# Kernel optimization log

Measured on AMD Instinct MI355X. Metric: run time of the kernel, lower is better.

## Reference

```python
import jax, jax.numpy as jnp
import numpy as np

TOP_K = 2  # routing_method: renormalize top-2 (topk then softmax over selected logits)


def setup_inputs() -> dict:
    key = jax.random.key(0)
    ks = jax.random.split(key, 5)
    T, H, I, E = 4096, 1024, 4096, 8
    return {
        "hidden_states": jax.random.normal(ks[0], (T, H), jnp.float32),
        "router_logits": jax.random.normal(ks[1], (T, E), jnp.float32),
        "W_gate": jax.random.normal(ks[2], (E, H, I), jnp.float32) * 0.02,  # w1
        "W_up": jax.random.normal(ks[3], (E, H, I), jnp.float32) * 0.02,   # w3
        "W_down": jax.random.normal(ks[4], (E, I, H), jnp.float32) * 0.02, # w2
    }


def reference(hidden_states, router_logits, W_gate, W_up, W_down):
    # Routing: top-k logits, renormalize with softmax over selected logits.
    top_vals, top_idx = jax.lax.top_k(router_logits, TOP_K)        # [T, K]
    routing_weights = jax.nn.softmax(top_vals, axis=-1)            # [T, K]

    E = W_gate.shape[0]
    out = jnp.zeros_like(hidden_states)                            # [T, H]
    for e in range(E):  # fixed small expert loop (structurally distinct weights)
        # combine weight for expert e per token (0 if not routed here)
        w_e = jnp.sum(jnp.where(top_idx == e, routing_weights, 0.0), axis=-1)  # [T]
        gate = hidden_states @ W_gate[e]                           # [T, I]
        up = hidden_states @ W_up[e]                               # [T, I]
        y = (jax.nn.silu(gate) * up) @ W_down[e]                   # [T, H]
        out = out + w_e[:, None] * y
    return out
```

## Files before the change

kernel.cpp:

```cpp
#include <hip/hip_runtime.h>

typedef float    f32x4 __attribute__((ext_vector_type(4)));
typedef _Float16 f16x8 __attribute__((ext_vector_type(8)));
typedef _Float16 f16x4 __attribute__((ext_vector_type(4)));

#define T_TOK 4096
#define HD    1024
#define ID    4096
#define NE    8
#define TOTP  (2*T_TOK)
#define MAXT1 72
#define MAXT2 40

#define WS_CNT   0
#define WS_FILL  64
#define WS_OFF   128
#define WS_TOT   192
#define WS_TOT2  196
#define WS_TEXP  256
#define WS_TM0   (256 + 4*MAXT1)
#define WS_TEXP2 (256 + 8*MAXT1)
#define WS_TM02  (256 + 8*MAXT1 + 4*MAXT2)
#define WS_TOPE  2048
#define WS_TOPW  (WS_TOPE + 4*TOTP)
#define WS_PAIR  (WS_TOPW + 4*TOTP)
#define WS_ACT   ((size_t)1 << 20)
constexpr size_t WS_YBUF = WS_ACT  + 2ull*TOTP*ID;
constexpr size_t WS_HS16 = WS_YBUF + 2ull*TOTP*HD;
constexpr size_t WS_WG16 = WS_HS16 + 2ull*T_TOK*HD;
constexpr size_t WS_WU16 = WS_WG16 + 2ull*NE*HD*ID;
constexpr size_t WS_WD16 = WS_WU16 + 2ull*NE*HD*ID;
constexpr size_t WS_YB   = WS_WG16;

__device__ __forceinline__ void gll16(const void* g, void* l) {
  __builtin_amdgcn_global_load_lds(
      (const __attribute__((address_space(1))) unsigned int*)g,
      (__attribute__((address_space(3))) unsigned int*)l, 16, 0, 0);
}

#define WAITV(N) do { \
    asm volatile("s_waitcnt vmcnt(" #N ")" ::: "memory"); \
    __builtin_amdgcn_sched_barrier(0); \
  } while (0)

__device__ __forceinline__ int lofs64(int row, int g8) {
  return row * 64 + ((g8 ^ (row & 7)) << 3);
}

__global__ void k_router(const float* __restrict__ logits, char* __restrict__ ws) {
  int t = blockIdx.x * blockDim.x + threadIdx.x;
  if (t >= T_TOK) return;
  float v0 = -1e30f, v1 = -1e30f; int i0 = 0, i1 = 0;
  #pragma unroll
  for (int e = 0; e < NE; ++e) {
    float v = logits[t * NE + e];
    if (v > v0)      { v1 = v0; i1 = i0; v0 = v; i0 = e; }
    else if (v > v1) { v1 = v;  i1 = e; }
  }
  float w0 = 1.f / (1.f + __expf(v1 - v0));
  ((int*)(ws + WS_TOPE))[2*t]   = i0;
  ((int*)(ws + WS_TOPE))[2*t+1] = i1;
  ((float*)(ws + WS_TOPW))[2*t]   = w0;
  ((float*)(ws + WS_TOPW))[2*t+1] = 1.f - w0;
  atomicAdd(&((int*)(ws + WS_CNT))[i0], 1);
  atomicAdd(&((int*)(ws + WS_CNT))[i1], 1);
}

__global__ void k_prefix(char* __restrict__ ws) {
  if (threadIdx.x != 0 || blockIdx.x != 0) return;
  const int* cnt = (const int*)(ws + WS_CNT);
  int* off   = (int*)(ws + WS_OFF);
  int* texp  = (int*)(ws + WS_TEXP);
  int* tm0   = (int*)(ws + WS_TM0);
  int* texp2 = (int*)(ws + WS_TEXP2);
  int* tm02  = (int*)(ws + WS_TM02);
  int run = 0, t1 = 0, t2 = 0;
  for (int e = 0; e < NE; ++e) {
    off[e] = run;
    int ne = cnt[e];
    for (int i = 0; i < ne; i += 128) { texp[t1] = e; tm0[t1] = i; ++t1; }
    for (int i = 0; i < ne; i += 256) { texp2[t2] = e; tm02[t2] = i; ++t2; }
    run += ne;
  }
  off[NE] = run;
  *(int*)(ws + WS_TOT)  = t1;
  *(int*)(ws + WS_TOT2) = t2;
}

__global__ void k_scatter(char* __restrict__ ws) {
  int t = blockIdx.x * blockDim.x + threadIdx.x;
  if (t >= T_TOK) return;
  const int* tope = (const int*)(ws + WS_TOPE);
  const int* off  = (const int*)(ws + WS_OFF);
  int* fill = (int*)(ws + WS_FILL);
  int* pair = (int*)(ws + WS_PAIR);
  #pragma unroll
  for (int s = 0; s < 2; ++s) {
    int id = 2*t + s;
    int e = tope[id];
    int pos = off[e] + atomicAdd(&fill[e], 1);
    pair[pos] = id;
  }
}

__global__ void k_hscvt(const float* __restrict__ src, _Float16* __restrict__ dst) {
  int i = blockIdx.x * blockDim.x + threadIdx.x;
  f32x4 v = ((const f32x4*)src)[i];
  f16x4 o;
  #pragma unroll
  for (int j = 0; j < 4; ++j) o[j] = (_Float16)v[j];
  ((f16x4*)dst)[i] = o;
}

__global__ __launch_bounds__(256) void k_wtrans(const float* __restrict__ src,
                                                _Float16* __restrict__ dst,
                                                int K, int N) {
  const int e = blockIdx.z;
  const int n0 = blockIdx.x * 64, k0 = blockIdx.y * 64;
  const float* s = src + (size_t)e * K * N;
  _Float16* d = dst + (size_t)e * (size_t)K * N;
  __shared__ _Float16 t[64][68];
  const int tx = threadIdx.x & 15, ty = threadIdx.x >> 4;
  #pragma unroll
  for (int it = 0; it < 4; ++it) {
    int k = k0 + it*16 + ty;
    f32x4 v = *(const f32x4*)&s[(size_t)k * N + n0 + tx*4];
    #pragma unroll
    for (int j = 0; j < 4; ++j) t[tx*4 + j][it*16 + ty] = (_Float16)v[j];
  }
  __syncthreads();
  #pragma unroll
  for (int it = 0; it < 4; ++it) {
    int n = it*16 + ty;
    *(f16x4*)&d[(size_t)(n0 + n) * K + k0 + tx*4] = *(const f16x4*)&t[n][tx*4];
  }
}

__global__ __launch_bounds__(512, 2) void k_gemm1(
    const _Float16* __restrict__ hs16, const _Float16* __restrict__ WgT,
    const _Float16* __restrict__ WuT, char* __restrict__ ws) {
  const int s = blockIdx.y;
  if (s >= *(const int*)(ws + WS_TOT2)) return;
  const int e    = ((const int*)(ws + WS_TEXP2))[s];
  const int m0   = ((const int*)(ws + WS_TM02))[s];
  const int offE = ((const int*)(ws + WS_OFF))[e];
  const int nE   = ((const int*)(ws + WS_CNT))[e];
  _Float16* __restrict__ act = (_Float16*)(ws + WS_ACT);
  const int n0 = blockIdx.x * 128;
  const int tid = threadIdx.x, lane = tid & 63, wid = tid >> 6;

  __shared__ __align__(16) _Float16 sm[2 * 32768];

  const int r8 = lane >> 3;
  const int q64 = (((lane & 7) ^ r8) << 3);
  const int* __restrict__ pairp = (const int*)(ws + WS_PAIR);
  const _Float16 *aP[4], *gP[2], *uP[2];
  #pragma unroll
  for (int c = 0; c < 4; ++c) {
    int mm = m0 + 32*wid + 8*c + r8;
    int tok = (mm < nE) ? (pairp[offE + mm] >> 1) : 0;
    aP[c] = hs16 + (size_t)tok * HD + q64;
  }
  #pragma unroll
  for (int c = 0; c < 2; ++c) {
    size_t col = (size_t)e * ID + (n0 + 16*wid + 8*c + r8);
    gP[c] = WgT + col * HD + q64;
    uP[c] = WuT + col * HD + q64;
  }

  auto stage8 = [&](int buf, int kt) {
    _Float16* base = sm + buf * 32768;
    const int ko = kt * 64;
    #pragma unroll
    for (int c = 0; c < 4; ++c)
      gll16(aP[c] + ko, base + (32*wid + 8*c) * 64);
    #pragma unroll
    for (int c = 0; c < 2; ++c) {
      gll16(gP[c] + ko, base + 16384 + (16*wid + 8*c) * 64);
      gll16(uP[c] + ko, base + 24576 + (16*wid + 8*c) * 64);
    }
  };

  const int wr = wid >> 2, wc = wid & 3;
  const int l15 = lane & 15, l4 = lane >> 4;
  f32x4 accg[8][2] = {}, accu[8][2] = {};

  auto computeKK = [&](int buf, int kk) {
    const _Float16* b0 = sm + buf * 32768;
    f16x8 afr[8], bg[2], bu[2];
    #pragma unroll
    for (int i = 0; i < 8; ++i) {
      const int row = 128*wr + 16*i + l15;
      afr[i] = *(const f16x8*)&b0[lofs64(row, kk*4 + l4)];
    }
    #pragma unroll
    for (int j = 0; j < 2; ++j) {
      const int row = 32*wc + 16*j + l15;
      bg[j] = *(const f16x8*)&b0[16384 + lofs64(row, kk*4 + l4)];
      bu[j] = *(const f16x8*)&b0[24576 + lofs64(row, kk*4 + l4)];
    }
    __builtin_amdgcn_s_setprio(1);
    #pragma unroll
    for (int i = 0; i < 8; ++i)
      #pragma unroll
      for (int j = 0; j < 2; ++j) {
        accg[i][j] = __builtin_amdgcn_mfma_f32_16x16x32_f16(afr[i], bg[j], accg[i][j], 0, 0, 0);
        accu[i][j] = __builtin_amdgcn_mfma_f32_16x16x32_f16(afr[i], bu[j], accu[i][j], 0, 0, 0);
      }
    __builtin_amdgcn_s_setprio(0);
  };

  const int KT = HD / 64;
  stage8(0, 0);
  WAITV(0);
  __builtin_amdgcn_s_barrier();
  for (int t = 0; t < KT; ++t) {
    const int cur = t & 1;
    if (t + 1 < KT) stage8(cur ^ 1, t + 1);
    computeKK(cur, 0);
    computeKK(cur, 1);
    WAITV(0);
    __builtin_amdgcn_s_barrier();
  }

  #pragma unroll
  for (int i = 0; i < 8; ++i)
    #pragma unroll
    for (int r = 0; r < 4; ++r) {
      const int mm = m0 + 128*wr + 16*i + 4*l4 + r;
      if (mm < nE) {
        const size_t prow = (size_t)(offE + mm) * ID;
        #pragma unroll
        for (int j = 0; j < 2; ++j) {
          float g = accg[i][j][r], u = accu[i][j][r];
          float sv = g / (1.f + __expf(-g)) * u;
          act[prow + n0 + 32*wc + 16*j + l15] = (_Float16)sv;
        }
      }
    }
}

__global__ __launch_bounds__(512, 2) void k_gemm2(const _Float16* __restrict__ WdT,
                                                  char* __restrict__ ws) {
  const int s = blockIdx.y;
  if (s >= *(const int*)(ws + WS_TOT2)) return;
  const int e    = ((const int*)(ws + WS_TEXP2))[s];
  const int m0   = ((const int*)(ws + WS_TM02))[s];
  const int offE = ((const int*)(ws + WS_OFF))[e];
  const int nE   = ((const int*)(ws + WS_CNT))[e];
  const int h    = blockIdx.z;
  const int kbase = h * (ID / 4);
  const int* __restrict__ pair = (const int*)(ws + WS_PAIR);
  const _Float16* __restrict__ act = (const _Float16*)(ws + WS_ACT);
  _Float16* __restrict__ yb = (_Float16*)(ws + WS_YB) + (size_t)h * TOTP * HD;
  const int n0 = blockIdx.x * 256;
  const int tid = threadIdx.x, lane = tid & 63, wid = tid >> 6;

  __shared__ __align__(16) _Float16 sm[2 * 32768];

  const int r8 = lane >> 3;
  const int q64 = (((lane & 7) ^ r8) << 3);
  const _Float16 *aP[4], *bP[4];
  #pragma unroll
  for (int c = 0; c < 4; ++c) {
    int mm = m0 + 32*wid + 8*c + r8;
    int p = (mm < nE) ? (offE + mm) : offE;
    aP[c] = act + (size_t)p * ID + kbase + q64;
  }
  #pragma unroll
  for (int c = 0; c < 4; ++c)
    bP[c] = WdT + ((size_t)e * HD + (n0 + 32*wid + 8*c + r8)) * ID + kbase + q64;

  auto stage8 = [&](int buf, int kt) {
    _Float16* base = sm + buf * 32768;
    const int ko = kt * 64;
    #pragma unroll
    for (int c = 0; c < 4; ++c)
      gll16(aP[c] + ko, base + (32*wid + 8*c) * 64);
    #pragma unroll
    for (int c = 0; c < 4; ++c)
      gll16(bP[c] + ko, base + 16384 + (32*wid + 8*c) * 64);
  };

  const int wr = wid >> 2, wc = wid & 3;
  const int l15 = lane & 15, l4 = lane >> 4;
  f32x4 acc[8][4] = {};

  auto computeKK = [&](int buf, int kk) {
    const _Float16* b0 = sm + buf * 32768;
    f16x8 afr[8], bfr[4];
    #pragma unroll
    for (int i = 0; i < 8; ++i)
      afr[i] = *(const f16x8*)&b0[lofs64(128*wr + 16*i + l15, kk*4 + l4)];
    #pragma unroll
    for (int j = 0; j < 4; ++j)
      bfr[j] = *(const f16x8*)&b0[16384 + lofs64(64*wc + 16*j + l15, kk*4 + l4)];
    __builtin_amdgcn_s_setprio(1);
    #pragma unroll
    for (int i = 0; i < 8; ++i)
      #pragma unroll
      for (int j = 0; j < 4; ++j)
        acc[i][j] = __builtin_amdgcn_mfma_f32_16x16x32_f16(afr[i], bfr[j], acc[i][j], 0, 0, 0);
    __builtin_amdgcn_s_setprio(0);
  };

  const int KT = (ID / 4) / 64;
  stage8(0, 0);
  WAITV(0);
  __builtin_amdgcn_s_barrier();
  for (int t = 0; t < KT; ++t) {
    const int cur = t & 1;
    if (t + 1 < KT) stage8(cur ^ 1, t + 1);
    computeKK(cur, 0);
    computeKK(cur, 1);
    WAITV(0);
    __builtin_amdgcn_s_barrier();
  }

  #pragma unroll
  for (int i = 0; i < 8; ++i)
    #pragma unroll
    for (int r = 0; r < 4; ++r) {
      const int mm = m0 + 128*wr + 16*i + 4*l4 + r;
      if (mm < nE) {
        const int id = pair[offE + mm];
        #pragma unroll
        for (int j = 0; j < 4; ++j)
          yb[(size_t)id * HD + n0 + 64*wc + 16*j + l15] = (_Float16)acc[i][j][r];
      }
    }
}

__global__ void k_combine(const char* __restrict__ ws, float* __restrict__ out) {
  const int idx = blockIdx.x * blockDim.x + threadIdx.x;
  const int t = idx >> 7, c = idx & 127;
  const float* topw = (const float*)(ws + WS_TOPW);
  const _Float16* yb = (const _Float16*)(ws + WS_YB);
  float s0[8] = {}, s1[8] = {};
  #pragma unroll
  for (int h = 0; h < 4; ++h) {
    const _Float16* p = yb + (size_t)h * TOTP * HD;
    f16x8 y0 = ((const f16x8*)(p + (size_t)(2*t)     * HD))[c];
    f16x8 y1 = ((const f16x8*)(p + (size_t)(2*t + 1) * HD))[c];
    #pragma unroll
    for (int j = 0; j < 8; ++j) { s0[j] += (float)y0[j]; s1[j] += (float)y1[j]; }
  }
  const float w0 = topw[2*t], w1 = topw[2*t+1];
  f32x4 o0, o1;
  #pragma unroll
  for (int j = 0; j < 4; ++j) {
    o0[j] = w0 * s0[j]     + w1 * s1[j];
    o1[j] = w0 * s0[4 + j] + w1 * s1[4 + j];
  }
  ((f32x4*)out)[2*idx]     = o0;
  ((f32x4*)out)[2*idx + 1] = o1;
}

extern "C" void kernel_launch(void* const* d_in, const int* in_sizes, int n_in,
                              void* d_out, int out_size, void* d_ws, size_t ws_size,
                              hipStream_t stream) {
  const float* hs     = (const float*)d_in[0];
  const float* logits = (const float*)d_in[1];
  const float* Wg     = (const float*)d_in[2];
  const float* Wu     = (const float*)d_in[3];
  const float* Wd     = (const float*)d_in[4];
  char* ws = (char*)d_ws;

  _Float16* hs16 = (_Float16*)(ws + WS_HS16);
  _Float16* wg16 = (_Float16*)(ws + WS_WG16);
  _Float16* wu16 = (_Float16*)(ws + WS_WU16);
  _Float16* wd16 = (_Float16*)(ws + WS_WD16);

  hipMemsetAsync(ws, 0, 256, stream);
  k_router <<<dim3(T_TOK/256), dim3(256), 0, stream>>>(logits, ws);
  k_prefix <<<dim3(1),         dim3(64),  0, stream>>>(ws);
  k_scatter<<<dim3(T_TOK/256), dim3(256), 0, stream>>>(ws);
  k_hscvt  <<<dim3(T_TOK*HD/4/256), dim3(256), 0, stream>>>(hs, hs16);
  k_wtrans <<<dim3(ID/64, HD/64, NE), dim3(256), 0, stream>>>(Wg, wg16, HD, ID);
  k_wtrans <<<dim3(ID/64, HD/64, NE), dim3(256), 0, stream>>>(Wu, wu16, HD, ID);
  k_wtrans <<<dim3(HD/64, ID/64, NE), dim3(256), 0, stream>>>(Wd, wd16, ID, HD);
  k_gemm1  <<<dim3(ID/128, MAXT2),    dim3(512), 0, stream>>>(hs16, wg16, wu16, ws);
  k_gemm2  <<<dim3(HD/256, MAXT2, 4), dim3(512), 0, stream>>>(wd16, ws);
  k_combine<<<dim3(T_TOK*HD/8/256), dim3(256), 0, stream>>>(ws, (float*)d_out);
}
```

Baseline: 479.9 us.

## Use 32x32x16 MFMA in both expert GEMMs and halve gemm2 split-K

Both grouped GEMMs switch from 16x16x32 to 32x32x16 f16 MFMA tiles, with new fragment loads and epilogue index mapping for the 32x32 accumulator layout. Each block keeps the same output tile but issues fewer, larger MFMAs and fewer LDS fragment reads. Separately, the down-projection split-K factor drops from 4 to 2. That halves the partial-result traffic written by gemm2 and read back by the combine kernel. The cost is half as many gemm2 blocks, which may leave some CUs underused, plus more accumulator registers per wave.

```diff
diff --git a/kernel.cpp b/kernel.cpp
--- a/kernel.cpp
+++ b/kernel.cpp
@@ -1,8 +1,9 @@
 #include <hip/hip_runtime.h>
 
-typedef float    f32x4 __attribute__((ext_vector_type(4)));
-typedef _Float16 f16x8 __attribute__((ext_vector_type(8)));
-typedef _Float16 f16x4 __attribute__((ext_vector_type(4)));
+typedef float    f32x4  __attribute__((ext_vector_type(4)));
+typedef float    f32x16 __attribute__((ext_vector_type(16)));
+typedef _Float16 f16x8  __attribute__((ext_vector_type(8)));
+typedef _Float16 f16x4  __attribute__((ext_vector_type(4)));
 
 #define T_TOK 4096
 #define HD    1024
@@ -182,31 +183,23 @@
   };
 
   const int wr = wid >> 2, wc = wid & 3;
-  const int l15 = lane & 15, l4 = lane >> 4;
-  f32x4 accg[8][2] = {}, accu[8][2] = {};
+  const int l31 = lane & 31, kh = lane >> 5;
+  f32x16 accg[4] = {}, accu[4] = {};
 
   auto computeKK = [&](int buf, int kk) {
     const _Float16* b0 = sm + buf * 32768;
-    f16x8 afr[8], bg[2], bu[2];
-    #pragma unroll
-    for (int i = 0; i < 8; ++i) {
-      const int row = 128*wr + 16*i + l15;
-      afr[i] = *(const f16x8*)&b0[lofs64(row, kk*4 + l4)];
+    f16x8 afr[4], bgf, buf_;
+    #pragma unroll
+    for (int i = 0; i < 4; ++i)
+      afr[i] = *(const f16x8*)&b0[lofs64(128*wr + 32*i + l31, kk*2 + kh)];
+    bgf  = *(const f16x8*)&b0[16384 + lofs64(32*wc + l31, kk*2 + kh)];
+    buf_ = *(const f16x8*)&b0[24576 + lofs64(32*wc + l31, kk*2 + kh)];
+    __builtin_amdgcn_s_setprio(1);
+    #pragma unroll
+    for (int i = 0; i < 4; ++i) {
+      accg[i] = __builtin_amdgcn_mfma_f32_32x32x16_f16(afr[i], bgf,  accg[i], 0, 0, 0);
+      accu[i] = __builtin_amdgcn_mfma_f32_32x32x16_f16(afr[i], buf_, accu[i], 0, 0, 0);
     }
-    #pragma unroll
-    for (int j = 0; j < 2; ++j) {
-      const int row = 32*wc + 16*j + l15;
-      bg[j] = *(const f16x8*)&b0[16384 + lofs64(row, kk*4 + l4)];
-      bu[j] = *(const f16x8*)&b0[24576 + lofs64(row, kk*4 + l4)];
-    }
-    __builtin_amdgcn_s_setprio(1);
-    #pragma unroll
-    for (int i = 0; i < 8; ++i)
-      #pragma unroll
-      for (int j = 0; j < 2; ++j) {
-        accg[i][j] = __builtin_amdgcn_mfma_f32_16x16x32_f16(afr[i], bg[j], accg[i][j], 0, 0, 0);
-        accu[i][j] = __builtin_amdgcn_mfma_f32_16x16x32_f16(afr[i], bu[j], accu[i][j], 0, 0, 0);
-      }
     __builtin_amdgcn_s_setprio(0);
   };
 
@@ -217,25 +210,22 @@
   for (int t = 0; t < KT; ++t) {
     const int cur = t & 1;
     if (t + 1 < KT) stage8(cur ^ 1, t + 1);
-    computeKK(cur, 0);
-    computeKK(cur, 1);
+    computeKK(cur, 0); computeKK(cur, 1);
+    computeKK(cur, 2); computeKK(cur, 3);
     WAITV(0);
     __builtin_amdgcn_s_barrier();
   }
 
   #pragma unroll
-  for (int i = 0; i < 8; ++i)
-    #pragma unroll
-    for (int r = 0; r < 4; ++r) {
-      const int mm = m0 + 128*wr + 16*i + 4*l4 + r;
+  for (int i = 0; i < 4; ++i)
+    #pragma unroll
+    for (int r = 0; r < 16; ++r) {
+      const int row = (r & 3) + 8 * (r >> 2) + 4 * kh;
+      const int mm = m0 + 128*wr + 32*i + row;
       if (mm < nE) {
-        const size_t prow = (size_t)(offE + mm) * ID;
-        #pragma unroll
-        for (int j = 0; j < 2; ++j) {
-          float g = accg[i][j][r], u = accu[i][j][r];
-          float sv = g / (1.f + __expf(-g)) * u;
-          act[prow + n0 + 32*wc + 16*j + l15] = (_Float16)sv;
-        }
+        float g = accg[i][r], u = accu[i][r];
+        float sv = g / (1.f + __expf(-g)) * u;
+        act[(size_t)(offE + mm) * ID + n0 + 32*wc + l31] = (_Float16)sv;
       }
     }
 }
@@ -249,7 +239,7 @@
   const int offE = ((const int*)(ws + WS_OFF))[e];
   const int nE   = ((const int*)(ws + WS_CNT))[e];
   const int h    = blockIdx.z;
-  const int kbase = h * (ID / 4);
+  const int kbase = h * (ID / 2);
   const int* __restrict__ pair = (const int*)(ws + WS_PAIR);
   const _Float16* __restrict__ act = (const _Float16*)(ws + WS_ACT);
   _Float16* __restrict__ yb = (_Float16*)(ws + WS_YB) + (size_t)h * TOTP * HD;
@@ -283,50 +273,51 @@
   };
 
   const int wr = wid >> 2, wc = wid & 3;
-  const int l15 = lane & 15, l4 = lane >> 4;
-  f32x4 acc[8][4] = {};
+  const int l31 = lane & 31, kh = lane >> 5;
+  f32x16 acc[4][2] = {};
 
   auto computeKK = [&](int buf, int kk) {
     const _Float16* b0 = sm + buf * 32768;
-    f16x8 afr[8], bfr[4];
-    #pragma unroll
-    for (int i = 0; i < 8; ++i)
-      afr[i] = *(const f16x8*)&b0[lofs64(128*wr + 16*i + l15, kk*4 + l4)];
-    #pragma unroll
-    for (int j = 0; j < 4; ++j)
-      bfr[j] = *(const f16x8*)&b0[16384 + lofs64(64*wc + 16*j + l15, kk*4 + l4)];
+    f16x8 afr[4], bfr[2];
+    #pragma unroll
+    for (int i = 0; i < 4; ++i)
+      afr[i] = *(const f16x8*)&b0[lofs64(128*wr + 32*i + l31, kk*2 + kh)];
+    #pragma unroll
+    for (int j = 0; j < 2; ++j)
+      bfr[j] = *(const f16x8*)&b0[16384 + lofs64(64*wc + 32*j + l31, kk*2 + kh)];
     __builtin_amdgcn_s_setprio(1);
     #pragma unroll
-    for (int i = 0; i < 8; ++i)
+    for (int i = 0; i < 4; ++i)
       #pragma unroll
-      for (int j = 0; j < 4; ++j)
-        acc[i][j] = __builtin_amdgcn_mfma_f32_16x16x32_f16(afr[i], bfr[j], acc[i][j], 0, 0, 0);
+      for (int j = 0; j < 2; ++j)
+        acc[i][j] = __builtin_amdgcn_mfma_f32_32x32x16_f16(afr[i], bfr[j], acc[i][j], 0, 0, 0);
     __builtin_amdgcn_s_setprio(0);
   };
 
-  const int KT = (ID / 4) / 64;
+  const int KT = (ID / 2) / 64;
   stage8(0, 0);
   WAITV(0);
   __builtin_amdgcn_s_barrier();
   for (int t = 0; t < KT; ++t) {
     const int cur = t & 1;
     if (t + 1 < KT) stage8(cur ^ 1, t + 1);
-    computeKK(cur, 0);
-    computeKK(cur, 1);
+    computeKK(cur, 0); computeKK(cur, 1);
+    computeKK(cur, 2); computeKK(cur, 3);
     WAITV(0);
     __builtin_amdgcn_s_barrier();
   }
 
   #pragma unroll
-  for (int i = 0; i < 8; ++i)
-    #pragma unroll
-    for (int r = 0; r < 4; ++r) {
-      const int mm = m0 + 128*wr + 16*i + 4*l4 + r;
+  for (int i = 0; i < 4; ++i)
+    #pragma unroll
+    for (int r = 0; r < 16; ++r) {
+      const int row = (r & 3) + 8 * (r >> 2) + 4 * kh;
+      const int mm = m0 + 128*wr + 32*i + row;
       if (mm < nE) {
         const int id = pair[offE + mm];
         #pragma unroll
-        for (int j = 0; j < 4; ++j)
-          yb[(size_t)id * HD + n0 + 64*wc + 16*j + l15] = (_Float16)acc[i][j][r];
+        for (int j = 0; j < 2; ++j)
+          yb[(size_t)id * HD + n0 + 64*wc + 32*j + l31] = (_Float16)acc[i][j][r];
       }
     }
 }
@@ -338,7 +329,7 @@
   const _Float16* yb = (const _Float16*)(ws + WS_YB);
   float s0[8] = {}, s1[8] = {};
   #pragma unroll
-  for (int h = 0; h < 4; ++h) {
+  for (int h = 0; h < 2; ++h) {
     const _Float16* p = yb + (size_t)h * TOTP * HD;
     f16x8 y0 = ((const f16x8*)(p + (size_t)(2*t)     * HD))[c];
     f16x8 y1 = ((const f16x8*)(p + (size_t)(2*t + 1) * HD))[c];
@@ -380,6 +371,6 @@
   k_wtrans <<<dim3(ID/64, HD/64, NE), dim3(256), 0, stream>>>(Wu, wu16, HD, ID);
   k_wtrans <<<dim3(HD/64, ID/64, NE), dim3(256), 0, stream>>>(Wd, wd16, ID, HD);
   k_gemm1  <<<dim3(ID/128, MAXT2),    dim3(512), 0, stream>>>(hs16, wg16, wu16, ws);
-  k_gemm2  <<<dim3(HD/256, MAXT2, 4), dim3(512), 0, stream>>>(wd16, ws);
+  k_gemm2  <<<dim3(HD/256, MAXT2, 2), dim3(512), 0, stream>>>(wd16, ws);
   k_combine<<<dim3(T_TOK*HD/8/256), dim3(256), 0, stream>>>(ws, (float*)d_out);
 }
```

Result: slower. 534.0 us (+11.3%).
